# Optimization experiments

Hardware: AMD Instinct MI355X
Metric: run time of the kernel (lower is better)

The kernel has to match this reference:

```python
import jax, jax.numpy as jnp
import numpy as np

B, S, D = 4, 2048, 4096
E, R, OUT = 4, 64, 4096
NUM_MOD, NUM_REG, HID = 4, 3, 128
ALPHA = 128.0
SCALING = ALPHA / R  # alpha / rank = 2.0
BALANCE_COEFF = 0.01


def setup_inputs() -> dict:
    key = jax.random.key(0)
    ks = jax.random.split(key, 8)
    return {
        "x": jax.random.normal(ks[0], (B, S, D), jnp.float32),
        "reliability_vec": jax.random.uniform(ks[1], (B, NUM_MOD), jnp.float32),
        "regime_vec": jax.random.uniform(ks[2], (B, NUM_REG), jnp.float32),
        # LoRA experts stacked: A ~ N(0, 1/rank), B random (torch inits B=0; randomized here for a non-trivial baseline)
        "lora_A": jax.random.normal(ks[3], (E, R, D), jnp.float32) / np.sqrt(R).astype(np.float32),
        "lora_B": jax.random.normal(ks[4], (E, OUT, R), jnp.float32) * 0.02,
        # router: Linear(4103->128) -> GELU -> Linear(128->4)
        "w1": jax.random.normal(ks[5], (D + NUM_MOD + NUM_REG, HID), jnp.float32) * 0.02,
        "b1": jnp.zeros((HID,), jnp.float32),
        "w2": jax.random.normal(ks[6], (HID, E), jnp.float32) * 0.02,
        "b2": jnp.zeros((E,), jnp.float32),
    }


def reference(x, reliability_vec, regime_vec, lora_A, lora_B, w1, b1, w2, b2):
    # Router on pooled features + degradation context
    x_pooled = x.mean(axis=1)                                   # [B, D]
    router_in = jnp.concatenate([x_pooled, reliability_vec, regime_vec], axis=-1)
    h = jax.nn.gelu(router_in @ w1 + b1)                        # [B, HID]
    gate_logits = h @ w2 + b2                                   # [B, E]
    gate_probs = jax.nn.softmax(gate_logits, axis=-1)
    top_expert = jnp.argmax(gate_probs, axis=-1)                # [B] int

    # Sparse top-1 dispatch (eval path): gather each sample's expert weights
    A_sel = lora_A[top_expert]                                  # [B, R, D]
    B_sel = lora_B[top_expert]                                  # [B, OUT, R]
    xr = jnp.einsum('bsd,brd->bsr', x, A_sel)                   # [B, S, R]
    out = jnp.einsum('bsr,bor->bso', xr, B_sel) * SCALING       # [B, S, OUT]

    avg_gate = gate_probs.mean(axis=0)
    balance_loss = BALANCE_COEFF * (E * jnp.sum(avg_gate ** 2))
    return out, balance_loss
```

## Files before the change

### kernel.cpp

```cpp
#include <hip/hip_runtime.h>

constexpr int B_ = 4, S_ = 2048, D_ = 4096, E_ = 4, R_ = 64, OUT_ = 4096;
constexpr int NMOD = 4, NREG = 3, HID_ = 128;
constexpr int RIN_ = D_ + NMOD + NREG;
constexpr float SCALING_ = 2.0f;
constexpr int SB_  = 64;
constexpr int NSB_ = S_ / SB_;
constexpr int KC_  = 33;

constexpr size_t WS_PP    = 0;
constexpr size_t WS_HACC2 = WS_PP + (size_t)NSB_ * B_ * D_;
constexpr size_t WS_TOP   = WS_HACC2 + B_ * KC_ * HID_;
constexpr size_t WS_ABF   = WS_TOP + 16;
constexpr size_t WS_BBF   = WS_ABF + (size_t)E_ * R_ * D_ / 2;
constexpr size_t WS_XRB   = WS_BBF + (size_t)E_ * OUT_ * R_ / 2;

using short8 = __attribute__((ext_vector_type(8))) short;
using f32x4  = __attribute__((ext_vector_type(4))) float;

__device__ inline unsigned short f2bf(float f) {
    unsigned u = __float_as_uint(f);
    unsigned r = u + 0x7FFFu + ((u >> 16) & 1u);
    return (unsigned short)(r >> 16);
}

__global__ void cvt_w_kernel(const float* __restrict__ A, const float* __restrict__ Bw,
                             ushort* __restrict__ Abf, ushort* __restrict__ Bbf) {
    int i = blockIdx.x * blockDim.x + threadIdx.x;
    constexpr int N4 = E_ * R_ * D_ / 4;
    if (i < N4) {
        float4 v = ((const float4*)A)[i];
        ((ushort4*)Abf)[i] = make_ushort4(f2bf(v.x), f2bf(v.y), f2bf(v.z), f2bf(v.w));
    } else {
        int j = i - N4;
        float4 v = ((const float4*)Bw)[j];
        ((ushort4*)Bbf)[j] = make_ushort4(f2bf(v.x), f2bf(v.y), f2bf(v.z), f2bf(v.w));
    }
}

__global__ __launch_bounds__(512, 4) void xe_kernel(const float* __restrict__ x,
                                                    const ushort* __restrict__ Abf,
                                                    float* __restrict__ pool_part,
                                                    ushort* __restrict__ xr_bf) {
    __shared__ ushort xs[SB_][72];
    __shared__ ushort as[R_][72];
    __shared__ float4 red2[8][16];
    int sb = blockIdx.x, b = blockIdx.y, e = blockIdx.z;
    int s0 = sb * SB_;
    int t = threadIdx.x, lane = t & 63, w = t >> 6;
    int m = w & 3, p = w >> 2;
    const float*  xb = x   + ((size_t)b * S_ + s0) * D_;
    const ushort* Ab = Abf + (size_t)e * R_ * D_;
    int xrow = t >> 4, xfq = t & 15;
    int arow = t >> 3, acq = t & 7;
    float4 v0 = *(const float4*)(xb + (size_t)xrow * D_ + xfq * 4);
    float4 v1 = *(const float4*)(xb + (size_t)(xrow + 32) * D_ + xfq * 4);
    int4  av  = *(const int4*)(Ab + (size_t)arow * D_ + acq * 8);
    f32x4 acc[2] = {};
    int mrow = m * 16 + (lane & 15);
    int koff = (lane >> 4) * 8;
    for (int kc = 0; kc < D_ / 64; ++kc) {
        __syncthreads();
        *(ushort4*)&xs[xrow][xfq * 4]      = make_ushort4(f2bf(v0.x), f2bf(v0.y), f2bf(v0.z), f2bf(v0.w));
        *(ushort4*)&xs[xrow + 32][xfq * 4] = make_ushort4(f2bf(v1.x), f2bf(v1.y), f2bf(v1.z), f2bf(v1.w));
        *(int4*)&as[arow][acq * 8] = av;
        if (e == 0) {
            float4 v = make_float4(v0.x + v1.x, v0.y + v1.y, v0.z + v1.z, v0.w + v1.w);
            v.x += __shfl_xor(v.x, 16); v.y += __shfl_xor(v.y, 16);
            v.z += __shfl_xor(v.z, 16); v.w += __shfl_xor(v.w, 16);
            v.x += __shfl_xor(v.x, 32); v.y += __shfl_xor(v.y, 32);
            v.z += __shfl_xor(v.z, 32); v.w += __shfl_xor(v.w, 32);
            if (lane < 16) red2[w][lane] = v;
        }
        __syncthreads();
        if (e == 0 && t < 16) {
            float4 s = red2[0][t];
#pragma unroll
            for (int j = 1; j < 8; ++j) {
                float4 r = red2[j][t];
                s.x += r.x; s.y += r.y; s.z += r.z; s.w += r.w;
            }
            *(float4*)&pool_part[(size_t)sb * (B_ * D_) + b * D_ + kc * 64 + t * 4] = s;
        }
        if (kc < D_ / 64 - 1) {
            int k0n = (kc + 1) * 64;
            v0 = *(const float4*)(xb + (size_t)xrow * D_ + k0n + xfq * 4);
            v1 = *(const float4*)(xb + (size_t)(xrow + 32) * D_ + k0n + xfq * 4);
            av = *(const int4*)(Ab + (size_t)arow * D_ + k0n + acq * 8);
        }
#pragma unroll
        for (int kk = 0; kk < 2; ++kk) {
            short8 af = *(const short8*)&xs[mrow][kk * 32 + koff];
#pragma unroll
            for (int n = 0; n < 2; ++n) {
                short8 bf = *(const short8*)&as[(p * 2 + n) * 16 + (lane & 15)][kk * 32 + koff];
                acc[n] = __builtin_amdgcn_mfma_f32_16x16x32_bf16(af, bf, acc[n], 0, 0, 0);
            }
        }
    }
    int col0 = lane & 15;
    int rb   = m * 16 + ((lane >> 4) << 2);
    ushort* xo = xr_bf + (((size_t)e * B_ + b) * S_ + s0) * R_;
#pragma unroll
    for (int n = 0; n < 2; ++n)
#pragma unroll
        for (int i = 0; i < 4; ++i)
            xo[(size_t)(rb + i) * R_ + (p * 2 + n) * 16 + col0] = f2bf(acc[n][i]);
}

__global__ __launch_bounds__(256) void router_h_kernel(const float* __restrict__ pool_part,
                                                       const float* __restrict__ rel,
                                                       const float* __restrict__ reg,
                                                       const float* __restrict__ w1,
                                                       float* __restrict__ hacc2) {
    __shared__ float rin[128];
    __shared__ float red[256];
    int b = blockIdx.x, kc = blockIdx.y;
    int t = threadIdx.x;
    int k0 = kc * 128;
    if (t < 128) {
        int k = k0 + t;
        float v = 0.f;
        if (k < D_) {
            float s = 0.f;
            for (int p = 0; p < NSB_; ++p) s += pool_part[(size_t)p * (B_ * D_) + b * D_ + k];
            v = s * (1.0f / S_);
        } else if (k < D_ + NMOD) v = rel[b * NMOD + (k - D_)];
        else if (k < RIN_)        v = reg[b * NREG + (k - D_ - NMOD)];
        rin[t] = v;
    }
    __syncthreads();
    int h = t & 127, half = t >> 7;
    float acc = 0.f;
#pragma unroll 8
    for (int i = 0; i < 64; ++i) {
        int kk = 2 * i + half;
        int k = k0 + kk;
        if (k < RIN_) acc += rin[kk] * w1[(size_t)k * HID_ + h];
    }
    red[t] = acc;
    __syncthreads();
    if (t < 128)
        hacc2[((size_t)b * KC_ + kc) * HID_ + t] = red[t] + red[t + 128];
}

__global__ void router_finish_kernel(const float* __restrict__ hacc2, const float* __restrict__ b1,
                                     const float* __restrict__ w2, const float* __restrict__ b2,
                                     int* __restrict__ top, float* __restrict__ bal_out) {
    __shared__ float h_lds[B_][HID_];
    __shared__ float logit[B_][E_];
    __shared__ float probs[B_][E_];
    int t = threadIdx.x;
    for (int b = 0; b < B_; ++b) {
        float v = b1[t];
        for (int j = 0; j < KC_; ++j) v += hacc2[((size_t)b * KC_ + j) * HID_ + t];
        float u = 0.7978845608028654f * (v + 0.044715f * v * v * v);
        h_lds[b][t] = 0.5f * v * (1.0f + tanhf(u));
    }
    __syncthreads();
    if (t < B_ * E_) {
        int b = t >> 2, e = t & 3;
        float acc = b2[e];
        for (int j = 0; j < HID_; ++j) acc += h_lds[b][j] * w2[j * E_ + e];
        logit[b][e] = acc;
    }
    __syncthreads();
    if (t < B_) {
        int b = t;
        float m = logit[b][0]; int arg = 0;
        for (int e = 1; e < E_; ++e) if (logit[b][e] > m) { m = logit[b][e]; arg = e; }
        float s = 0.f, p[E_];
        for (int e = 0; e < E_; ++e) { p[e] = expf(logit[b][e] - m); s += p[e]; }
        for (int e = 0; e < E_; ++e) probs[b][e] = p[e] / s;
        top[b] = arg;
    }
    __syncthreads();
    if (t == 0) {
        float bal = 0.f;
        for (int e = 0; e < E_; ++e) {
            float avg = 0.25f * (probs[0][e] + probs[1][e] + probs[2][e] + probs[3][e]);
            bal += avg * avg;
        }
        *bal_out = 0.01f * E_ * bal;
    }
}

__global__ __launch_bounds__(256) void out_kernel(const ushort* __restrict__ xr_bf,
                                                  const ushort* __restrict__ Bbf,
                                                  const int* __restrict__ top,
                                                  float* __restrict__ out) {
    __shared__ ushort xrs[64][72];
    __shared__ ushort bs[128][72];
    int b  = blockIdx.z;
    int e  = top[b];
    int s0 = blockIdx.x * 64, o0 = blockIdx.y * 128;
    int t = threadIdx.x, lane = t & 63, w = t >> 6;
    const ushort* xrb = xr_bf + (((size_t)e * B_ + b) * S_ + s0) * R_;
#pragma unroll
    for (int i = 0; i < 2; ++i) {
        int lin = t + 256 * i; int row = lin >> 3, cq = lin & 7;
        int4 v = *(const int4*)(xrb + (size_t)row * R_ + cq * 8);
        *(int4*)&xrs[row][cq * 8] = v;
    }
    const ushort* Bb = Bbf + (size_t)e * OUT_ * R_ + (size_t)o0 * R_;
#pragma unroll
    for (int i = 0; i < 4; ++i) {
        int lin = t + 256 * i; int row = lin >> 3, cq = lin & 7;
        int4 v = *(const int4*)(Bb + (size_t)row * R_ + cq * 8);
        *(int4*)&bs[row][cq * 8] = v;
    }
    __syncthreads();
    int mrow = w * 16 + (lane & 15);
    int koff = (lane >> 4) * 8;
    f32x4 acc[8] = {};
#pragma unroll
    for (int kk = 0; kk < 2; ++kk) {
        short8 af = *(const short8*)&xrs[mrow][kk * 32 + koff];
#pragma unroll
        for (int n = 0; n < 8; ++n) {
            short8 bf = *(const short8*)&bs[n * 16 + (lane & 15)][kk * 32 + koff];
            acc[n] = __builtin_amdgcn_mfma_f32_16x16x32_bf16(af, bf, acc[n], 0, 0, 0);
        }
    }
    int col0  = lane & 15;
    int rbase = (lane >> 4) << 2;
    float* ob = out + ((size_t)b * S_ + s0 + w * 16) * OUT_ + o0;
#pragma unroll
    for (int n = 0; n < 8; ++n)
#pragma unroll
        for (int i = 0; i < 4; ++i)
            ob[(size_t)(rbase + i) * OUT_ + n * 16 + col0] = acc[n][i] * SCALING_;
}

extern "C" void kernel_launch(void* const* d_in, const int* in_sizes, int n_in,
                              void* d_out, int out_size, void* d_ws, size_t ws_size,
                              hipStream_t stream) {
    const float* x   = (const float*)d_in[0];
    const float* rel = (const float*)d_in[1];
    const float* reg = (const float*)d_in[2];
    const float* lA  = (const float*)d_in[3];
    const float* lB  = (const float*)d_in[4];
    const float* w1  = (const float*)d_in[5];
    const float* b1  = (const float*)d_in[6];
    const float* w2  = (const float*)d_in[7];
    const float* b2  = (const float*)d_in[8];
    float* out = (float*)d_out;
    float* ws  = (float*)d_ws;

    float*  pp    = ws + WS_PP;
    float*  hacc2 = ws + WS_HACC2;
    int*    top   = (int*)(ws + WS_TOP);
    ushort* Abf   = (ushort*)(ws + WS_ABF);
    ushort* Bbf   = (ushort*)(ws + WS_BBF);
    ushort* xrb   = (ushort*)(ws + WS_XRB);

    cvt_w_kernel<<<2 * (E_ * R_ * D_ / 4) / 256, 256, 0, stream>>>(lA, lB, Abf, Bbf);
    xe_kernel<<<dim3(NSB_, B_, E_), 512, 0, stream>>>(x, Abf, pp, xrb);
    router_h_kernel<<<dim3(B_, KC_), 256, 0, stream>>>(pp, rel, reg, w1, hacc2);
    router_finish_kernel<<<1, 128, 0, stream>>>(hacc2, b1, w2, b2, top,
                                                out + (size_t)out_size - 1);
    out_kernel<<<dim3(S_ / 64, OUT_ / 128, B_), 256, 0, stream>>>(xrb, Bbf, top, out);
}
```

Baseline: 133.3 us.

## Pre-convert x to bf16 with fused pooling, then run the projection on bf16

A new kernel reads fp32 x once, writes a bf16 copy and computes partial sums for the mean-pool. The projection kernel then loads bf16 x for each expert instead of re-reading fp32 x and converting it four times. The projection kernel also moves to 128-wide K chunks and drops its in-loop pooling reduction. In exchange it adds a 64 MB bf16 write, an extra launch and larger shared-memory tiles with lower occupancy bounds.

New measurement: 157.5 us. +18.1%, slower.

```diff
diff --git a/kernel.cpp b/kernel.cpp
--- a/kernel.cpp
+++ b/kernel.cpp
@@ -4,8 +4,7 @@
 constexpr int NMOD = 4, NREG = 3, HID_ = 128;
 constexpr int RIN_ = D_ + NMOD + NREG;
 constexpr float SCALING_ = 2.0f;
-constexpr int SB_  = 64;
-constexpr int NSB_ = S_ / SB_;
+constexpr int NSB_ = 128;
 constexpr int KC_  = 33;
 
 constexpr size_t WS_PP    = 0;
@@ -14,6 +13,7 @@
 constexpr size_t WS_ABF   = WS_TOP + 16;
 constexpr size_t WS_BBF   = WS_ABF + (size_t)E_ * R_ * D_ / 2;
 constexpr size_t WS_XRB   = WS_BBF + (size_t)E_ * OUT_ * R_ / 2;
+constexpr size_t WS_XBF   = WS_XRB + (size_t)E_ * B_ * S_ * R_ / 2;
 
 using short8 = __attribute__((ext_vector_type(8))) short;
 using f32x4  = __attribute__((ext_vector_type(4))) float;
@@ -38,62 +38,68 @@
     }
 }
 
-__global__ __launch_bounds__(512, 4) void xe_kernel(const float* __restrict__ x,
+__global__ __launch_bounds__(512) void cvtx_pool_kernel(const float* __restrict__ x,
+                                                        ushort* __restrict__ xbf,
+                                                        float* __restrict__ pp) {
+    int sb = blockIdx.x, b = blockIdx.y;
+    int s0 = sb * 16;
+    int t = threadIdx.x;
+    const float4* xp = (const float4*)(x + ((size_t)b * S_ + s0) * D_);
+    ushort4*      xo = (ushort4*)(xbf + ((size_t)b * S_ + s0) * D_);
+    float4 a0 = {0.f, 0.f, 0.f, 0.f}, a1 = {0.f, 0.f, 0.f, 0.f};
+#pragma unroll 4
+    for (int r = 0; r < 16; ++r) {
+        float4 v0 = xp[(size_t)r * 1024 + t];
+        float4 v1 = xp[(size_t)r * 1024 + t + 512];
+        a0.x += v0.x; a0.y += v0.y; a0.z += v0.z; a0.w += v0.w;
+        a1.x += v1.x; a1.y += v1.y; a1.z += v1.z; a1.w += v1.w;
+        xo[(size_t)r * 1024 + t]       = make_ushort4(f2bf(v0.x), f2bf(v0.y), f2bf(v0.z), f2bf(v0.w));
+        xo[(size_t)r * 1024 + t + 512] = make_ushort4(f2bf(v1.x), f2bf(v1.y), f2bf(v1.z), f2bf(v1.w));
+    }
+    float* ppb = pp + ((size_t)sb * B_ + b) * D_;
+    *(float4*)&ppb[t * 4]         = a0;
+    *(float4*)&ppb[(t + 512) * 4] = a1;
+}
+
+__global__ __launch_bounds__(512, 2) void xe_kernel(const ushort* __restrict__ xbf,
                                                     const ushort* __restrict__ Abf,
-                                                    float* __restrict__ pool_part,
                                                     ushort* __restrict__ xr_bf) {
-    __shared__ ushort xs[SB_][72];
-    __shared__ ushort as[R_][72];
-    __shared__ float4 red2[8][16];
+    __shared__ ushort xs[64][136];
+    __shared__ ushort as[64][136];
     int sb = blockIdx.x, b = blockIdx.y, e = blockIdx.z;
-    int s0 = sb * SB_;
+    int s0 = sb * 64;
     int t = threadIdx.x, lane = t & 63, w = t >> 6;
     int m = w & 3, p = w >> 2;
-    const float*  xb = x   + ((size_t)b * S_ + s0) * D_;
+    const ushort* xb = xbf + ((size_t)b * S_ + s0) * D_;
     const ushort* Ab = Abf + (size_t)e * R_ * D_;
-    int xrow = t >> 4, xfq = t & 15;
-    int arow = t >> 3, acq = t & 7;
-    float4 v0 = *(const float4*)(xb + (size_t)xrow * D_ + xfq * 4);
-    float4 v1 = *(const float4*)(xb + (size_t)(xrow + 32) * D_ + xfq * 4);
-    int4  av  = *(const int4*)(Ab + (size_t)arow * D_ + acq * 8);
+    int r0 = t >> 4, oc = t & 15;
+    int4 xv0 = *(const int4*)(xb + (size_t)r0 * D_ + oc * 8);
+    int4 xv1 = *(const int4*)(xb + (size_t)(r0 + 32) * D_ + oc * 8);
+    int4 av0 = *(const int4*)(Ab + (size_t)r0 * D_ + oc * 8);
+    int4 av1 = *(const int4*)(Ab + (size_t)(r0 + 32) * D_ + oc * 8);
     f32x4 acc[2] = {};
     int mrow = m * 16 + (lane & 15);
     int koff = (lane >> 4) * 8;
-    for (int kc = 0; kc < D_ / 64; ++kc) {
+    for (int kc = 0; kc < D_ / 128; ++kc) {
         __syncthreads();
-        *(ushort4*)&xs[xrow][xfq * 4]      = make_ushort4(f2bf(v0.x), f2bf(v0.y), f2bf(v0.z), f2bf(v0.w));
-        *(ushort4*)&xs[xrow + 32][xfq * 4] = make_ushort4(f2bf(v1.x), f2bf(v1.y), f2bf(v1.z), f2bf(v1.w));
-        *(int4*)&as[arow][acq * 8] = av;
-        if (e == 0) {
-            float4 v = make_float4(v0.x + v1.x, v0.y + v1.y, v0.z + v1.z, v0.w + v1.w);
-            v.x += __shfl_xor(v.x, 16); v.y += __shfl_xor(v.y, 16);
-            v.z += __shfl_xor(v.z, 16); v.w += __shfl_xor(v.w, 16);
-            v.x += __shfl_xor(v.x, 32); v.y += __shfl_xor(v.y, 32);
-            v.z += __shfl_xor(v.z, 32); v.w += __shfl_xor(v.w, 32);
-            if (lane < 16) red2[w][lane] = v;
-        }
+        *(int4*)&xs[r0][oc * 8]      = xv0;
+        *(int4*)&xs[r0 + 32][oc * 8] = xv1;
+        *(int4*)&as[r0][oc * 8]      = av0;
+        *(int4*)&as[r0 + 32][oc * 8] = av1;
         __syncthreads();
-        if (e == 0 && t < 16) {
-            float4 s = red2[0][t];
-#pragma unroll
-            for (int j = 1; j < 8; ++j) {
-                float4 r = red2[j][t];
-                s.x += r.x; s.y += r.y; s.z += r.z; s.w += r.w;
-            }
-            *(float4*)&pool_part[(size_t)sb * (B_ * D_) + b * D_ + kc * 64 + t * 4] = s;
-        }
-        if (kc < D_ / 64 - 1) {
-            int k0n = (kc + 1) * 64;
-            v0 = *(const float4*)(xb + (size_t)xrow * D_ + k0n + xfq * 4);
-            v1 = *(const float4*)(xb + (size_t)(xrow + 32) * D_ + k0n + xfq * 4);
-            av = *(const int4*)(Ab + (size_t)arow * D_ + k0n + acq * 8);
-        }
-#pragma unroll
-        for (int kk = 0; kk < 2; ++kk) {
-            short8 af = *(const short8*)&xs[mrow][kk * 32 + koff];
+        if (kc < D_ / 128 - 1) {
+            int k0 = (kc + 1) * 128;
+            xv0 = *(const int4*)(xb + (size_t)r0 * D_ + k0 + oc * 8);
+            xv1 = *(const int4*)(xb + (size_t)(r0 + 32) * D_ + k0 + oc * 8);
+            av0 = *(const int4*)(Ab + (size_t)r0 * D_ + k0 + oc * 8);
+            av1 = *(const int4*)(Ab + (size_t)(r0 + 32) * D_ + k0 + oc * 8);
+        }
+#pragma unroll
+        for (int kf = 0; kf < 4; ++kf) {
+            short8 af = *(const short8*)&xs[mrow][kf * 32 + koff];
 #pragma unroll
             for (int n = 0; n < 2; ++n) {
-                short8 bf = *(const short8*)&as[(p * 2 + n) * 16 + (lane & 15)][kk * 32 + koff];
+                short8 bf = *(const short8*)&as[(p * 2 + n) * 16 + (lane & 15)][kf * 32 + koff];
                 acc[n] = __builtin_amdgcn_mfma_f32_16x16x32_bf16(af, bf, acc[n], 0, 0, 0);
             }
         }
@@ -108,7 +114,7 @@
             xo[(size_t)(rb + i) * R_ + (p * 2 + n) * 16 + col0] = f2bf(acc[n][i]);
 }
 
-__global__ __launch_bounds__(256) void router_h_kernel(const float* __restrict__ pool_part,
+__global__ __launch_bounds__(256) void router_h_kernel(const float* __restrict__ pp,
                                                        const float* __restrict__ rel,
                                                        const float* __restrict__ reg,
                                                        const float* __restrict__ w1,
@@ -123,7 +129,7 @@
         float v = 0.f;
         if (k < D_) {
             float s = 0.f;
-            for (int p = 0; p < NSB_; ++p) s += pool_part[(size_t)p * (B_ * D_) + b * D_ + k];
+            for (int pi = 0; pi < NSB_; ++pi) s += pp[((size_t)pi * B_ + b) * D_ + k];
             v = s * (1.0f / S_);
         } else if (k < D_ + NMOD) v = rel[b * NMOD + (k - D_)];
         else if (k < RIN_)        v = reg[b * NREG + (k - D_ - NMOD)];
@@ -169,9 +175,9 @@
         int b = t;
         float m = logit[b][0]; int arg = 0;
         for (int e = 1; e < E_; ++e) if (logit[b][e] > m) { m = logit[b][e]; arg = e; }
-        float s = 0.f, p[E_];
-        for (int e = 0; e < E_; ++e) { p[e] = expf(logit[b][e] - m); s += p[e]; }
-        for (int e = 0; e < E_; ++e) probs[b][e] = p[e] / s;
+        float s = 0.f, pv[E_];
+        for (int e = 0; e < E_; ++e) { pv[e] = expf(logit[b][e] - m); s += pv[e]; }
+        for (int e = 0; e < E_; ++e) probs[b][e] = pv[e] / s;
         top[b] = arg;
     }
     __syncthreads();
@@ -253,9 +259,11 @@
     ushort* Abf   = (ushort*)(ws + WS_ABF);
     ushort* Bbf   = (ushort*)(ws + WS_BBF);
     ushort* xrb   = (ushort*)(ws + WS_XRB);
+    ushort* xbf   = (ushort*)(ws + WS_XBF);
 
     cvt_w_kernel<<<2 * (E_ * R_ * D_ / 4) / 256, 256, 0, stream>>>(lA, lB, Abf, Bbf);
-    xe_kernel<<<dim3(NSB_, B_, E_), 512, 0, stream>>>(x, Abf, pp, xrb);
+    cvtx_pool_kernel<<<dim3(NSB_, B_), 512, 0, stream>>>(x, xbf, pp);
+    xe_kernel<<<dim3(S_ / 64, B_, E_), 512, 0, stream>>>(xbf, Abf, xrb);
     router_h_kernel<<<dim3(B_, KC_), 256, 0, stream>>>(pp, rel, reg, w1, hacc2);
     router_finish_kernel<<<1, 128, 0, stream>>>(hacc2, b1, w2, b2, top,
                                                 out + (size_t)out_size - 1);
```

## Shrink xe tiles, move pooling to a prologue split across expert blocks

Applied to the files above, without the earlier changes.

The x·A projection kernel now works on 32-row tiles with 256 threads, which doubles the grid. Mean pooling is taken out of the main loop: each expert block sums an 8-row slice of x in a prologue and writes its own partial, so expert-0 blocks no longer carry the extra shuffle and reduction work. The router then reduces four times as many partials, with both halves of the block sharing that work. LDS row padding drops from 72 to 70 elements in both GEMM kernels. The trade-offs are an extra pass over x for pooling, a larger partials buffer, and LDS rows that are no longer 16-byte aligned for the vector accesses.

Measured after the change: 211.9 us. 1.59x slower.

```diff
diff --git a/kernel.cpp b/kernel.cpp
--- a/kernel.cpp
+++ b/kernel.cpp
@@ -4,12 +4,12 @@
 constexpr int NMOD = 4, NREG = 3, HID_ = 128;
 constexpr int RIN_ = D_ + NMOD + NREG;
 constexpr float SCALING_ = 2.0f;
-constexpr int SB_  = 64;
-constexpr int NSB_ = S_ / SB_;
+constexpr int NSB_ = 64;
+constexpr int P_   = NSB_ * E_;
 constexpr int KC_  = 33;
 
 constexpr size_t WS_PP    = 0;
-constexpr size_t WS_HACC2 = WS_PP + (size_t)NSB_ * B_ * D_;
+constexpr size_t WS_HACC2 = WS_PP + (size_t)P_ * B_ * D_;
 constexpr size_t WS_TOP   = WS_HACC2 + B_ * KC_ * HID_;
 constexpr size_t WS_ABF   = WS_TOP + 16;
 constexpr size_t WS_BBF   = WS_ABF + (size_t)E_ * R_ * D_ / 2;
@@ -38,55 +38,62 @@
     }
 }
 
-__global__ __launch_bounds__(512, 4) void xe_kernel(const float* __restrict__ x,
+__global__ __launch_bounds__(256, 4) void xe_kernel(const float* __restrict__ x,
                                                     const ushort* __restrict__ Abf,
-                                                    float* __restrict__ pool_part,
+                                                    float* __restrict__ pp,
                                                     ushort* __restrict__ xr_bf) {
-    __shared__ ushort xs[SB_][72];
-    __shared__ ushort as[R_][72];
-    __shared__ float4 red2[8][16];
+    __shared__ ushort xs[32][70];
+    __shared__ ushort as[64][70];
     int sb = blockIdx.x, b = blockIdx.y, e = blockIdx.z;
-    int s0 = sb * SB_;
+    int s0 = sb * 32;
     int t = threadIdx.x, lane = t & 63, w = t >> 6;
-    int m = w & 3, p = w >> 2;
+    int m = w & 1, p = w >> 1;
+
+    {
+        const float4* xp = (const float4*)(x + ((size_t)b * S_ + s0 + e * 8) * D_);
+        float4 a0 = {0,0,0,0}, a1 = {0,0,0,0}, a2 = {0,0,0,0}, a3 = {0,0,0,0};
+#pragma unroll
+        for (int r = 0; r < 8; ++r) {
+            float4 v0 = xp[(size_t)r * 1024 + t];
+            float4 v1 = xp[(size_t)r * 1024 + 256 + t];
+            float4 v2 = xp[(size_t)r * 1024 + 512 + t];
+            float4 v3 = xp[(size_t)r * 1024 + 768 + t];
+            a0.x += v0.x; a0.y += v0.y; a0.z += v0.z; a0.w += v0.w;
+            a1.x += v1.x; a1.y += v1.y; a1.z += v1.z; a1.w += v1.w;
+            a2.x += v2.x; a2.y += v2.y; a2.z += v2.z; a2.w += v2.w;
+            a3.x += v3.x; a3.y += v3.y; a3.z += v3.z; a3.w += v3.w;
+        }
+        float* ppb = pp + ((size_t)(sb * E_ + e) * B_ + b) * D_;
+        *(float4*)&ppb[(t)       * 4] = a0;
+        *(float4*)&ppb[(256 + t) * 4] = a1;
+        *(float4*)&ppb[(512 + t) * 4] = a2;
+        *(float4*)&ppb[(768 + t) * 4] = a3;
+    }
+
     const float*  xb = x   + ((size_t)b * S_ + s0) * D_;
     const ushort* Ab = Abf + (size_t)e * R_ * D_;
-    int xrow = t >> 4, xfq = t & 15;
-    int arow = t >> 3, acq = t & 7;
-    float4 v0 = *(const float4*)(xb + (size_t)xrow * D_ + xfq * 4);
-    float4 v1 = *(const float4*)(xb + (size_t)(xrow + 32) * D_ + xfq * 4);
-    int4  av  = *(const int4*)(Ab + (size_t)arow * D_ + acq * 8);
+    int xr_ = t >> 3, xc = t & 7;
+    int ar  = t >> 2, ac = (t & 3) * 2;
+    float4 xv0 = *(const float4*)(xb + (size_t)xr_ * D_ + xc * 8);
+    float4 xv1 = *(const float4*)(xb + (size_t)xr_ * D_ + xc * 8 + 4);
+    int4   av0 = *(const int4*)(Ab + (size_t)ar * D_ + ac * 8);
+    int4   av1 = *(const int4*)(Ab + (size_t)ar * D_ + (ac + 1) * 8);
     f32x4 acc[2] = {};
     int mrow = m * 16 + (lane & 15);
     int koff = (lane >> 4) * 8;
     for (int kc = 0; kc < D_ / 64; ++kc) {
         __syncthreads();
-        *(ushort4*)&xs[xrow][xfq * 4]      = make_ushort4(f2bf(v0.x), f2bf(v0.y), f2bf(v0.z), f2bf(v0.w));
-        *(ushort4*)&xs[xrow + 32][xfq * 4] = make_ushort4(f2bf(v1.x), f2bf(v1.y), f2bf(v1.z), f2bf(v1.w));
-        *(int4*)&as[arow][acq * 8] = av;
-        if (e == 0) {
-            float4 v = make_float4(v0.x + v1.x, v0.y + v1.y, v0.z + v1.z, v0.w + v1.w);
-            v.x += __shfl_xor(v.x, 16); v.y += __shfl_xor(v.y, 16);
-            v.z += __shfl_xor(v.z, 16); v.w += __shfl_xor(v.w, 16);
-            v.x += __shfl_xor(v.x, 32); v.y += __shfl_xor(v.y, 32);
-            v.z += __shfl_xor(v.z, 32); v.w += __shfl_xor(v.w, 32);
-            if (lane < 16) red2[w][lane] = v;
-        }
+        *(ushort4*)&xs[xr_][xc * 8]     = make_ushort4(f2bf(xv0.x), f2bf(xv0.y), f2bf(xv0.z), f2bf(xv0.w));
+        *(ushort4*)&xs[xr_][xc * 8 + 4] = make_ushort4(f2bf(xv1.x), f2bf(xv1.y), f2bf(xv1.z), f2bf(xv1.w));
+        *(int4*)&as[ar][ac * 8]         = av0;
+        *(int4*)&as[ar][(ac + 1) * 8]   = av1;
         __syncthreads();
-        if (e == 0 && t < 16) {
-            float4 s = red2[0][t];
-#pragma unroll
-            for (int j = 1; j < 8; ++j) {
-                float4 r = red2[j][t];
-                s.x += r.x; s.y += r.y; s.z += r.z; s.w += r.w;
-            }
-            *(float4*)&pool_part[(size_t)sb * (B_ * D_) + b * D_ + kc * 64 + t * 4] = s;
-        }
         if (kc < D_ / 64 - 1) {
-            int k0n = (kc + 1) * 64;
-            v0 = *(const float4*)(xb + (size_t)xrow * D_ + k0n + xfq * 4);
-            v1 = *(const float4*)(xb + (size_t)(xrow + 32) * D_ + k0n + xfq * 4);
-            av = *(const int4*)(Ab + (size_t)arow * D_ + k0n + acq * 8);
+            int k0 = (kc + 1) * 64;
+            xv0 = *(const float4*)(xb + (size_t)xr_ * D_ + k0 + xc * 8);
+            xv1 = *(const float4*)(xb + (size_t)xr_ * D_ + k0 + xc * 8 + 4);
+            av0 = *(const int4*)(Ab + (size_t)ar * D_ + k0 + ac * 8);
+            av1 = *(const int4*)(Ab + (size_t)ar * D_ + k0 + (ac + 1) * 8);
         }
 #pragma unroll
         for (int kk = 0; kk < 2; ++kk) {
@@ -108,7 +115,7 @@
             xo[(size_t)(rb + i) * R_ + (p * 2 + n) * 16 + col0] = f2bf(acc[n][i]);
 }
 
-__global__ __launch_bounds__(256) void router_h_kernel(const float* __restrict__ pool_part,
+__global__ __launch_bounds__(256) void router_h_kernel(const float* __restrict__ pp,
                                                        const float* __restrict__ rel,
                                                        const float* __restrict__ reg,
                                                        const float* __restrict__ w1,
@@ -118,14 +125,21 @@
     int b = blockIdx.x, kc = blockIdx.y;
     int t = threadIdx.x;
     int k0 = kc * 128;
+    {
+        int k = k0 + (t & 127), half = t >> 7;
+        float s = 0.f;
+        if (k < D_) {
+            for (int pi = half * (P_ / 2); pi < (half + 1) * (P_ / 2); ++pi)
+                s += pp[((size_t)pi * B_ + b) * D_ + k];
+        }
+        red[t] = s;
+    }
+    __syncthreads();
     if (t < 128) {
         int k = k0 + t;
         float v = 0.f;
-        if (k < D_) {
-            float s = 0.f;
-            for (int p = 0; p < NSB_; ++p) s += pool_part[(size_t)p * (B_ * D_) + b * D_ + k];
-            v = s * (1.0f / S_);
-        } else if (k < D_ + NMOD) v = rel[b * NMOD + (k - D_)];
+        if (k < D_)               v = (red[t] + red[t + 128]) * (1.0f / S_);
+        else if (k < D_ + NMOD)   v = rel[b * NMOD + (k - D_)];
         else if (k < RIN_)        v = reg[b * NREG + (k - D_ - NMOD)];
         rin[t] = v;
     }
@@ -167,11 +181,11 @@
     __syncthreads();
     if (t < B_) {
         int b = t;
-        float m = logit[b][0]; int arg = 0;
-        for (int e = 1; e < E_; ++e) if (logit[b][e] > m) { m = logit[b][e]; arg = e; }
-        float s = 0.f, p[E_];
-        for (int e = 0; e < E_; ++e) { p[e] = expf(logit[b][e] - m); s += p[e]; }
-        for (int e = 0; e < E_; ++e) probs[b][e] = p[e] / s;
+        float mx = logit[b][0]; int arg = 0;
+        for (int e = 1; e < E_; ++e) if (logit[b][e] > mx) { mx = logit[b][e]; arg = e; }
+        float s = 0.f, pv[E_];
+        for (int e = 0; e < E_; ++e) { pv[e] = expf(logit[b][e] - mx); s += pv[e]; }
+        for (int e = 0; e < E_; ++e) probs[b][e] = pv[e] / s;
         top[b] = arg;
     }
     __syncthreads();
@@ -189,8 +203,8 @@
                                                   const ushort* __restrict__ Bbf,
                                                   const int* __restrict__ top,
                                                   float* __restrict__ out) {
-    __shared__ ushort xrs[64][72];
-    __shared__ ushort bs[128][72];
+    __shared__ ushort xrs[64][70];
+    __shared__ ushort bs[128][70];
     int b  = blockIdx.z;
     int e  = top[b];
     int s0 = blockIdx.x * 64, o0 = blockIdx.y * 128;
@@ -255,7 +269,7 @@
     ushort* xrb   = (ushort*)(ws + WS_XRB);
 
     cvt_w_kernel<<<2 * (E_ * R_ * D_ / 4) / 256, 256, 0, stream>>>(lA, lB, Abf, Bbf);
-    xe_kernel<<<dim3(NSB_, B_, E_), 512, 0, stream>>>(x, Abf, pp, xrb);
+    xe_kernel<<<dim3(NSB_, B_, E_), 256, 0, stream>>>(x, Abf, pp, xrb);
     router_h_kernel<<<dim3(B_, KC_), 256, 0, stream>>>(pp, rel, reg, w1, hacc2);
     router_finish_kernel<<<1, 128, 0, stream>>>(hacc2, b1, w2, b2, top,
                                                 out + (size_t)out_size - 1);
```
